# Kernel optimization log

Hardware: AMD Instinct MI355X
Metric: run time of the kernel (lower is better)

## Reference

```python
import jax, jax.numpy as jnp
import numpy as np

B, T, C, H = 2, 2048, 2048, 16  # batch, seq_len, dim, num_heads
D = C // H  # head_dim = 128
ROPE_BASE = 10000.0


def apply_rope(x, pos):
    # x: [B, T, H, D]; adjacent-pair rotation (torchtune convention)
    d = x.shape[-1]
    inv_freq = 1.0 / (ROPE_BASE ** (jnp.arange(0, d, 2, dtype=jnp.float32) / d))  # [D/2]
    freqs = pos.astype(jnp.float32)[:, None] * inv_freq[None, :]                 # [T, D/2]
    cos = jnp.cos(freqs)[None, :, None, :]
    sin = jnp.sin(freqs)[None, :, None, :]
    x1 = x[..., 0::2]
    x2 = x[..., 1::2]
    out = jnp.stack([x1 * cos - x2 * sin, x2 * cos + x1 * sin], axis=-1)  # [B,T,H,D/2,2]
    return out.reshape(x.shape)


def setup_inputs() -> dict:
    key = jax.random.key(0)
    k1, k2, k3 = jax.random.split(key, 3)
    x = jax.random.normal(k1, (B, T, C), dtype=jnp.float32)
    # 0.02 init scale keeps attention logits in a sane range
    W_qkv = jax.random.normal(k2, (C, 3 * C), dtype=jnp.float32) * 0.02
    W_out = jax.random.normal(k3, (C, C), dtype=jnp.float32) * 0.02
    return {"x": x, "W_qkv": W_qkv, "W_out": W_out}


def reference(x, W_qkv, W_out):
    b, t, c = x.shape
    h, d = H, c // H
    # fused QKV projection
    qkv = (x @ W_qkv).reshape(b, t, 3, h, d)
    q, k, v = qkv[:, :, 0], qkv[:, :, 1], qkv[:, :, 2]  # [B,T,H,D] each
    pos = jnp.arange(t)  # cache_pos = 0 (prefill)
    q = apply_rope(q, pos)
    k = apply_rope(k, pos)
    scale = 1.0 / np.sqrt(d).astype(np.float32)
    scores = jnp.einsum('bqhd,bkhd->bhqk', q, k) * scale  # [B,H,T,T]
    causal = jnp.tril(jnp.ones((t, t), dtype=bool))
    scores = jnp.where(causal[None, None], scores, -jnp.inf)
    probs = jax.nn.softmax(scores, axis=-1)
    o = jnp.einsum('bhqk,bkhd->bqhd', probs, v).reshape(b, t, c)
    return o @ W_out
```

## Files before the change

### kernel.cpp

```cpp
#include <hip/hip_runtime.h>
#include <stdint.h>

#define TSEQ 2048

typedef __bf16 bf16x8 __attribute__((ext_vector_type(8)));
typedef float f32x4 __attribute__((ext_vector_type(4)));

typedef const __attribute__((address_space(1))) unsigned int* gas_u32;
typedef __attribute__((address_space(3))) unsigned int* las_u32;

__device__ __forceinline__ f32x4 mfma16(bf16x8 a, bf16x8 b, f32x4 c) {
  return __builtin_amdgcn_mfma_f32_16x16x32_bf16(a, b, c, 0, 0, 0);
}

__device__ __forceinline__ unsigned short f2b(float f) {
  unsigned int u = __float_as_uint(f);
  u += 0x7fffu + ((u >> 16) & 1u);
  return (unsigned short)(u >> 16);
}

__device__ __forceinline__ void gload_lds16(const unsigned short* g, unsigned short* l) {
  __builtin_amdgcn_global_load_lds((gas_u32)(const void*)g, (las_u32)(void*)l, 16, 0, 0);
}

__global__ __launch_bounds__(256) void cast_bf16_kernel(const float* __restrict__ src,
                                                        unsigned short* __restrict__ dst) {
  size_t i = ((size_t)blockIdx.x * 256 + threadIdx.x) * 4;
  float4 v = *(const float4*)(src + i);
  ushort4 o;
  o.x = f2b(v.x); o.y = f2b(v.y); o.z = f2b(v.z); o.w = f2b(v.w);
  *(ushort4*)(dst + i) = o;
}

__global__ __launch_bounds__(256) void transpose_cast_kernel(const float* __restrict__ src,
                                                             unsigned short* __restrict__ dst,
                                                             int R, int Cc) {
  __shared__ float tile[64][65];
  int cb = blockIdx.x * 64;
  int rb = blockIdx.y * 64;
  int t = threadIdx.x;
  int tr = t >> 4;
  int tc = (t & 15) * 4;
#pragma unroll
  for (int i = 0; i < 4; i++) {
    int r = tr + 16 * i;
    float4 v = *(const float4*)(src + (size_t)(rb + r) * Cc + cb + tc);
    tile[r][tc + 0] = v.x; tile[r][tc + 1] = v.y;
    tile[r][tc + 2] = v.z; tile[r][tc + 3] = v.w;
  }
  __syncthreads();
#pragma unroll
  for (int i = 0; i < 4; i++) {
    int r2 = tr + 16 * i;
    ushort4 o;
    o.x = f2b(tile[tc + 0][r2]);
    o.y = f2b(tile[tc + 1][r2]);
    o.z = f2b(tile[tc + 2][r2]);
    o.w = f2b(tile[tc + 3][r2]);
    *(ushort4*)(dst + (size_t)(cb + r2) * R + rb + tc) = o;
  }
}

__device__ __forceinline__ void gemm_bt_core(const unsigned short* __restrict__ A,
                                             const unsigned short* __restrict__ Bt,
                                             int K, int bm, int bn,
                                             unsigned short* sA, unsigned short* sB,
                                             f32x4 (&acc)[4][4]) {
  const int t = threadIdx.x;
  const int lane = t & 63, w = t >> 6;
  const int wm = (w >> 1) * 64, wn = (w & 1) * 64;
  const int quad = lane >> 4, l16 = lane & 15;

  const int r0 = t >> 2, s0 = (t & 3) * 8;
  const int r1 = r0 + 64;
  const unsigned short* Arow0 = A + (size_t)(bm + r0) * K + s0;
  const unsigned short* Arow1 = A + (size_t)(bm + r1) * K + s0;
  const unsigned short* Brow0 = Bt + (size_t)(bn + r0) * K + s0;
  const unsigned short* Brow1 = Bt + (size_t)(bn + r1) * K + s0;
  unsigned short* sA0 = sA + t * 8;
  unsigned short* sA1 = sA + (t + 256) * 8;
  unsigned short* sB0 = sB + t * 8;
  unsigned short* sB1 = sB + (t + 256) * 8;

#pragma unroll 1
  for (int k0 = 0; k0 < K; k0 += 32) {
    gload_lds16(Arow0 + k0, sA0);
    gload_lds16(Arow1 + k0, sA1);
    gload_lds16(Brow0 + k0, sB0);
    gload_lds16(Brow1 + k0, sB1);
    __syncthreads();
    bf16x8 a[4], b[4];
#pragma unroll
    for (int i = 0; i < 4; i++)
      a[i] = *(const bf16x8*)(sA + (wm + i * 16 + l16) * 32 + quad * 8);
#pragma unroll
    for (int j = 0; j < 4; j++)
      b[j] = *(const bf16x8*)(sB + (wn + j * 16 + l16) * 32 + quad * 8);
#pragma unroll
    for (int i = 0; i < 4; i++)
#pragma unroll
      for (int j = 0; j < 4; j++)
        acc[i][j] = mfma16(a[i], b[j], acc[i][j]);
    __syncthreads();
  }
}

__global__ __launch_bounds__(256) void gemm_qkv_rope(const unsigned short* __restrict__ Xb,
                                                     const unsigned short* __restrict__ Wqt,
                                                     unsigned short* __restrict__ Qd,
                                                     unsigned short* __restrict__ Kd,
                                                     unsigned short* __restrict__ Vtd) {
  __shared__ unsigned short smem[128 * 136];
  unsigned short* sA = smem;
  unsigned short* sB = smem + 4096;
  f32x4 acc[4][4];
  const f32x4 z = {0.f, 0.f, 0.f, 0.f};
#pragma unroll
  for (int i = 0; i < 4; i++)
#pragma unroll
    for (int j = 0; j < 4; j++) acc[i][j] = z;

  const int bm = blockIdx.y * 128;
  const int bnb = blockIdx.x;
  gemm_bt_core(Xb, Wqt, 2048, bm, bnb * 128, sA, sB, acc);

  const int s = bnb >> 4, h = bnb & 15;
  const int t = threadIdx.x, lane = t & 63, w = t >> 6;
  const int wm = (w >> 1) * 64, wn = (w & 1) * 64;
  const int quad = lane >> 4, l16 = lane & 15;
  const int bq = bm >> 11;
  const int tpos0 = bm & (TSEQ - 1);
  unsigned short* sC = smem;

  if (s < 2) {
    const float scl = (s == 0) ? 0.08838834764831845f : 1.0f;
#pragma unroll
    for (int j = 0; j < 4; j++) {
      int d = wn + j * 16 + l16;
      float invf = __expf(-(float)(d >> 1) * 0.14391157f);
#pragma unroll
      for (int i = 0; i < 4; i++) {
#pragma unroll
        for (int r = 0; r < 4; r++) {
          int row = wm + i * 16 + quad * 4 + r;
          float ang = (float)(tpos0 + row) * invf;
          float sn, cs;
          __sincosf(ang, &sn, &cs);
          float v = acc[i][j][r];
          float p = __shfl_xor(v, 1, 64);
          float outv = (d & 1) ? (v * cs + p * sn) : (v * cs - p * sn);
          sC[row * 136 + d] = f2b(outv * scl);
        }
      }
    }
    __syncthreads();
    unsigned short* dst = (s == 0) ? Qd : Kd;
    size_t gbase = ((size_t)(bq * 16 + h) * TSEQ + tpos0) * 128;
#pragma unroll
    for (int it = 0; it < 8; it++) {
      int c = t + 256 * it;
      int row = c >> 4, off = (c & 15) * 8;
      uint4 vv = *(const uint4*)(sC + row * 136 + off);
      *(uint4*)(dst + gbase + (size_t)row * 128 + off) = vv;
    }
  } else {
#pragma unroll
    for (int j = 0; j < 4; j++) {
      int d = wn + j * 16 + l16;
#pragma unroll
      for (int i = 0; i < 4; i++)
#pragma unroll
        for (int r = 0; r < 4; r++) {
          int col = wm + i * 16 + quad * 4 + r;
          sC[d * 136 + col] = f2b(acc[i][j][r]);
        }
    }
    __syncthreads();
    size_t gbase = ((size_t)(bq * 16 + h) * 128) * TSEQ + tpos0;
#pragma unroll
    for (int it = 0; it < 8; it++) {
      int c = t + 256 * it;
      int row = c >> 4, off = (c & 15) * 8;
      uint4 vv = *(const uint4*)(sC + row * 136 + off);
      *(uint4*)(Vtd + gbase + (size_t)row * TSEQ + off) = vv;
    }
  }
}

__global__ __launch_bounds__(256, 2) void attn_kernel(const unsigned short* __restrict__ Q,
                                                      const unsigned short* __restrict__ Kmat,
                                                      const unsigned short* __restrict__ Vt,
                                                      unsigned short* __restrict__ Ob) {
  __shared__ unsigned short smem[37376];
  const int pair = blockIdx.x, bh = blockIdx.y;
  const int qA = pair, qB = 31 - pair;
  const int t = threadIdx.x, lane = t & 63, w = t >> 6, quad = lane >> 4, l16 = lane & 15;
  const size_t base = (size_t)bh * TSEQ * 128;
  const unsigned short* Qp = Q + base;
  const unsigned short* Kp = Kmat + base;
  const unsigned short* Vp = Vt + base;
  unsigned short* myP = smem + 32768 + w * 1152;

  bf16x8 aqA[4], aqB[4];
  {
    int qrA = qA * 64 + w * 16 + l16;
    int qrB = qB * 64 + w * 16 + l16;
#pragma unroll
    for (int kk = 0; kk < 4; kk++) {
      aqA[kk] = *(const bf16x8*)(Qp + (size_t)qrA * 128 + kk * 32 + quad * 8);
      aqB[kk] = *(const bf16x8*)(Qp + (size_t)qrB * 128 + kk * 32 + quad * 8);
    }
  }
  const f32x4 z = {0.f, 0.f, 0.f, 0.f};
  f32x4 oA[8], oB[8];
  float mA[4], lA[4], mB[4], lB[4];
#pragma unroll
  for (int dt = 0; dt < 8; dt++) { oA[dt] = z; oB[dt] = z; }
#pragma unroll
  for (int r = 0; r < 4; r++) { mA[r] = -1e30f; lA[r] = 0.f; mB[r] = -1e30f; lB[r] = 0.f; }

  auto load_tiles = [&](int kb, int buf) {
    unsigned short* bK = smem + buf * 16384;
    unsigned short* bV = bK + 8192;
    const unsigned short* Kt = Kp + (size_t)kb * 64 * 128;
#pragma unroll
    for (int i2 = 0; i2 < 4; i2++) {
      int idx = t + 256 * i2;
      int r = idx >> 4, cS = idx & 15;
      int c = cS ^ (r & 7);
      gload_lds16(Kt + r * 128 + c * 8, bK + idx * 8);
    }
#pragma unroll
    for (int i2 = 0; i2 < 4; i2++) {
      int idx = t + 256 * i2;
      int r = idx >> 3, cS = idx & 7;
      int c = cS ^ (r & 7);
      gload_lds16(Vp + (size_t)r * TSEQ + kb * 64 + c * 8, bV + idx * 8);
    }
  };

  auto process = [&](bf16x8 (&aq)[4], f32x4 (&o)[8], float (&mst)[4], float (&lst)[4],
                     int qb, int kb, const unsigned short* bK, const unsigned short* bV) {
    f32x4 S[4];
#pragma unroll
    for (int nt = 0; nt < 4; nt++) {
      f32x4 sacc = z;
#pragma unroll
      for (int kk = 0; kk < 4; kk++) {
        const unsigned short* p =
            bK + (nt * 16 + l16) * 128 + (((kk * 4 + quad) ^ (l16 & 7)) * 8);
        sacc = mfma16(aq[kk], *(const bf16x8*)p, sacc);
      }
      S[nt] = sacc;
    }
    if (kb == qb) {
      int qg = qb * 64 + w * 16 + quad * 4;
#pragma unroll
      for (int nt = 0; nt < 4; nt++) {
        int key = kb * 64 + nt * 16 + l16;
#pragma unroll
        for (int r = 0; r < 4; r++)
          if (key > qg + r) S[nt][r] = -1e30f;
      }
    }
    float alpha[4];
#pragma unroll
    for (int r = 0; r < 4; r++) {
      float mx = fmaxf(fmaxf(S[0][r], S[1][r]), fmaxf(S[2][r], S[3][r]));
      mx = fmaxf(mx, __shfl_xor(mx, 1, 64));
      mx = fmaxf(mx, __shfl_xor(mx, 2, 64));
      mx = fmaxf(mx, __shfl_xor(mx, 4, 64));
      mx = fmaxf(mx, __shfl_xor(mx, 8, 64));
      float mnew = fmaxf(mst[r], mx);
      alpha[r] = __expf(mst[r] - mnew);
      mst[r] = mnew;
    }
    float rs[4] = {0.f, 0.f, 0.f, 0.f};
#pragma unroll
    for (int nt = 0; nt < 4; nt++)
#pragma unroll
      for (int r = 0; r < 4; r++) {
        float p = __expf(S[nt][r] - mst[r]);
        S[nt][r] = p;
        rs[r] += p;
      }
#pragma unroll
    for (int r = 0; r < 4; r++) {
      float s4 = rs[r];
      s4 += __shfl_xor(s4, 1, 64);
      s4 += __shfl_xor(s4, 2, 64);
      s4 += __shfl_xor(s4, 4, 64);
      s4 += __shfl_xor(s4, 8, 64);
      lst[r] = lst[r] * alpha[r] + s4;
#pragma unroll
      for (int nt = 0; nt < 4; nt++)
        myP[(quad * 4 + r) * 72 + nt * 16 + l16] = f2b(S[nt][r]);
    }
#pragma unroll
    for (int dt = 0; dt < 8; dt++) {
      f32x4 ov = o[dt];
      ov[0] *= alpha[0]; ov[1] *= alpha[1]; ov[2] *= alpha[2]; ov[3] *= alpha[3];
      o[dt] = ov;
    }
#pragma unroll
    for (int kk = 0; kk < 2; kk++) {
      bf16x8 ap = *(const bf16x8*)(myP + l16 * 72 + kk * 32 + quad * 8);
#pragma unroll
      for (int dt = 0; dt < 8; dt++) {
        const unsigned short* p =
            bV + (dt * 16 + l16) * 64 + (((kk * 4 + quad) ^ (l16 & 7)) * 8);
        o[dt] = mfma16(ap, *(const bf16x8*)p, o[dt]);
      }
    }
  };

  load_tiles(0, 0);
#pragma unroll 1
  for (int kb = 0; kb <= qB; kb++) {
    __syncthreads();
    if (kb < qB) load_tiles(kb + 1, (kb + 1) & 1);
    const unsigned short* bK = smem + (kb & 1) * 16384;
    const unsigned short* bV = bK + 8192;
    process(aqB, oB, mB, lB, qB, kb, bK, bV);
    if (kb <= qA) process(aqA, oA, mA, lA, qA, kb, bK, bV);
  }

  __syncthreads();
  unsigned short* sOA = smem;
  unsigned short* sOB = smem + 8704;
#pragma unroll
  for (int dt = 0; dt < 8; dt++)
#pragma unroll
    for (int r = 0; r < 4; r++) {
      int row = w * 16 + quad * 4 + r;
      sOA[row * 136 + dt * 16 + l16] = f2b(oA[dt][r] / lA[r]);
      sOB[row * 136 + dt * 16 + l16] = f2b(oB[dt][r] / lB[r]);
    }
  __syncthreads();
  const int b = bh >> 4, h = bh & 15;
#pragma unroll
  for (int it = 0; it < 4; it++) {
    int c = t + 256 * it;
    int row = c >> 4, off = (c & 15) * 8;
    uint4 va = *(const uint4*)(sOA + row * 136 + off);
    *(uint4*)(Ob + (size_t)(b * TSEQ + qA * 64 + row) * 2048 + h * 128 + off) = va;
    uint4 vb = *(const uint4*)(sOB + row * 136 + off);
    *(uint4*)(Ob + (size_t)(b * TSEQ + qB * 64 + row) * 2048 + h * 128 + off) = vb;
  }
}

__global__ __launch_bounds__(256) void gemm_out_kernel(const unsigned short* __restrict__ Ob,
                                                       const unsigned short* __restrict__ Wot,
                                                       float* __restrict__ Cout) {
  __shared__ unsigned short sA[128 * 32];
  __shared__ unsigned short sB[128 * 32];
  f32x4 acc[4][4];
  const f32x4 z = {0.f, 0.f, 0.f, 0.f};
#pragma unroll
  for (int i = 0; i < 4; i++)
#pragma unroll
    for (int j = 0; j < 4; j++) acc[i][j] = z;

  const int bm = blockIdx.y * 128, bn = blockIdx.x * 128;
  gemm_bt_core(Ob, Wot, 2048, bm, bn, sA, sB, acc);

  const int t = threadIdx.x, lane = t & 63, w = t >> 6;
  const int wm = (w >> 1) * 64, wn = (w & 1) * 64;
  const int quad = lane >> 4, l16 = lane & 15;
#pragma unroll
  for (int i = 0; i < 4; i++)
#pragma unroll
    for (int j = 0; j < 4; j++)
#pragma unroll
      for (int r = 0; r < 4; r++) {
        int row = bm + wm + i * 16 + quad * 4 + r;
        int col = bn + wn + j * 16 + l16;
        Cout[(size_t)row * 2048 + col] = acc[i][j][r];
      }
}

extern "C" void kernel_launch(void* const* d_in, const int* in_sizes, int n_in,
                              void* d_out, int out_size, void* d_ws, size_t ws_size,
                              hipStream_t stream) {
  (void)in_sizes; (void)n_in; (void)out_size; (void)ws_size;
  const float* x = (const float*)d_in[0];
  const float* Wqkv = (const float*)d_in[1];
  const float* Wout = (const float*)d_in[2];
  float* out = (float*)d_out;
  char* ws = (char*)d_ws;

  unsigned short* Xb  = (unsigned short*)(ws);
  unsigned short* Wqt = (unsigned short*)(ws + 16777216);
  unsigned short* Wot = (unsigned short*)(ws + 41943040);
  unsigned short* Qd  = (unsigned short*)(ws + 50331648);
  unsigned short* Kd  = (unsigned short*)(ws + 67108864);
  unsigned short* Vtd = (unsigned short*)(ws + 83886080);
  unsigned short* Obf = (unsigned short*)(ws + 100663296);

  cast_bf16_kernel<<<8192, 256, 0, stream>>>(x, Xb);
  transpose_cast_kernel<<<dim3(96, 32), 256, 0, stream>>>(Wqkv, Wqt, 2048, 6144);
  transpose_cast_kernel<<<dim3(32, 32), 256, 0, stream>>>(Wout, Wot, 2048, 2048);
  gemm_qkv_rope<<<dim3(48, 32), 256, 0, stream>>>(Xb, Wqt, Qd, Kd, Vtd);
  attn_kernel<<<dim3(16, 32), 256, 0, stream>>>(Qd, Kd, Vtd, Obf);
  gemm_out_kernel<<<dim3(16, 32), 256, 0, stream>>>(Obf, Wot, out);
}
```

Before: 441.2 us.

## Double-buffer LDS in GEMM core to overlap global loads with MFMA

Replaces the single-buffered GEMM main loop with a two-stage LDS ring. The next K-slice is issued via global_load_lds before the current slice's MFMAs, which removes one barrier per iteration and hides load latency. It also adds launch_bounds occupancy hints of 4 blocks per CU to both GEMM kernels. The cost is doubled LDS per block, and the occupancy hint may force register pressure or spills.

New measurement: 403.6 us. 1.09x faster.

```diff
diff --git a/kernel.cpp b/kernel.cpp
--- a/kernel.cpp
+++ b/kernel.cpp
@@ -61,34 +61,39 @@
   }
 }
 
-__device__ __forceinline__ void gemm_bt_core(const unsigned short* __restrict__ A,
-                                             const unsigned short* __restrict__ Bt,
-                                             int K, int bm, int bn,
-                                             unsigned short* sA, unsigned short* sB,
-                                             f32x4 (&acc)[4][4]) {
+__device__ __forceinline__ void gemm_bt_core_db(const unsigned short* __restrict__ A,
+                                                const unsigned short* __restrict__ Bt,
+                                                int K, int bm, int bn,
+                                                unsigned short* sm,
+                                                f32x4 (&acc)[4][4]) {
   const int t = threadIdx.x;
   const int lane = t & 63, w = t >> 6;
   const int wm = (w >> 1) * 64, wn = (w & 1) * 64;
   const int quad = lane >> 4, l16 = lane & 15;
 
   const int r0 = t >> 2, s0 = (t & 3) * 8;
-  const int r1 = r0 + 64;
   const unsigned short* Arow0 = A + (size_t)(bm + r0) * K + s0;
-  const unsigned short* Arow1 = A + (size_t)(bm + r1) * K + s0;
+  const unsigned short* Arow1 = Arow0 + (size_t)64 * K;
   const unsigned short* Brow0 = Bt + (size_t)(bn + r0) * K + s0;
-  const unsigned short* Brow1 = Bt + (size_t)(bn + r1) * K + s0;
-  unsigned short* sA0 = sA + t * 8;
-  unsigned short* sA1 = sA + (t + 256) * 8;
-  unsigned short* sB0 = sB + t * 8;
-  unsigned short* sB1 = sB + (t + 256) * 8;
-
+  const unsigned short* Brow1 = Brow0 + (size_t)64 * K;
+
+  auto stage = [&](int k0, int buf) {
+    unsigned short* sA = sm + buf * 8192;
+    unsigned short* sB = sA + 4096;
+    gload_lds16(Arow0 + k0, sA + t * 8);
+    gload_lds16(Arow1 + k0, sA + (t + 256) * 8);
+    gload_lds16(Brow0 + k0, sB + t * 8);
+    gload_lds16(Brow1 + k0, sB + (t + 256) * 8);
+  };
+
+  stage(0, 0);
+  const int nIter = K >> 5;
 #pragma unroll 1
-  for (int k0 = 0; k0 < K; k0 += 32) {
-    gload_lds16(Arow0 + k0, sA0);
-    gload_lds16(Arow1 + k0, sA1);
-    gload_lds16(Brow0 + k0, sB0);
-    gload_lds16(Brow1 + k0, sB1);
+  for (int it = 0; it < nIter; it++) {
     __syncthreads();
+    if (it + 1 < nIter) stage((it + 1) * 32, (it + 1) & 1);
+    const unsigned short* sA = sm + (it & 1) * 8192;
+    const unsigned short* sB = sA + 4096;
     bf16x8 a[4], b[4];
 #pragma unroll
     for (int i = 0; i < 4; i++)
@@ -101,18 +106,16 @@
 #pragma unroll
       for (int j = 0; j < 4; j++)
         acc[i][j] = mfma16(a[i], b[j], acc[i][j]);
-    __syncthreads();
-  }
-}
-
-__global__ __launch_bounds__(256) void gemm_qkv_rope(const unsigned short* __restrict__ Xb,
-                                                     const unsigned short* __restrict__ Wqt,
-                                                     unsigned short* __restrict__ Qd,
-                                                     unsigned short* __restrict__ Kd,
-                                                     unsigned short* __restrict__ Vtd) {
-  __shared__ unsigned short smem[128 * 136];
-  unsigned short* sA = smem;
-  unsigned short* sB = smem + 4096;
+  }
+  __syncthreads();
+}
+
+__global__ __launch_bounds__(256, 4) void gemm_qkv_rope(const unsigned short* __restrict__ Xb,
+                                                        const unsigned short* __restrict__ Wqt,
+                                                        unsigned short* __restrict__ Qd,
+                                                        unsigned short* __restrict__ Kd,
+                                                        unsigned short* __restrict__ Vtd) {
+  __shared__ unsigned short smem[17408];
   f32x4 acc[4][4];
   const f32x4 z = {0.f, 0.f, 0.f, 0.f};
 #pragma unroll
@@ -122,7 +125,7 @@
 
   const int bm = blockIdx.y * 128;
   const int bnb = blockIdx.x;
-  gemm_bt_core(Xb, Wqt, 2048, bm, bnb * 128, sA, sB, acc);
+  gemm_bt_core_db(Xb, Wqt, 2048, bm, bnb * 128, smem, acc);
 
   const int s = bnb >> 4, h = bnb & 15;
   const int t = threadIdx.x, lane = t & 63, w = t >> 6;
@@ -349,11 +352,10 @@
   }
 }
 
-__global__ __launch_bounds__(256) void gemm_out_kernel(const unsigned short* __restrict__ Ob,
-                                                       const unsigned short* __restrict__ Wot,
-                                                       float* __restrict__ Cout) {
-  __shared__ unsigned short sA[128 * 32];
-  __shared__ unsigned short sB[128 * 32];
+__global__ __launch_bounds__(256, 4) void gemm_out_kernel(const unsigned short* __restrict__ Ob,
+                                                          const unsigned short* __restrict__ Wot,
+                                                          float* __restrict__ Cout) {
+  __shared__ unsigned short smem[16384];
   f32x4 acc[4][4];
   const f32x4 z = {0.f, 0.f, 0.f, 0.f};
 #pragma unroll
@@ -362,7 +364,7 @@
     for (int j = 0; j < 4; j++) acc[i][j] = z;
 
   const int bm = blockIdx.y * 128, bn = blockIdx.x * 128;
-  gemm_bt_core(Ob, Wot, 2048, bm, bn, sA, sB, acc);
+  gemm_bt_core_db(Ob, Wot, 2048, bm, bn, smem, acc);
 
   const int t = threadIdx.x, lane = t & 63, w = t >> 6;
   const int wm = (w >> 1) * 64, wn = (w & 1) * 64;
```
